# Performance work log

Hardware: AMD Instinct MI355X
Metric: run time of the kernel (lower is better)

## Reference

```python
import jax, jax.numpy as jnp
import numpy as np

# Grid shapes derived from video (T=30, H=720, W=1280), grid_size=8, n_levels=2:
# level i: ceil([T,H,W] / 8 / 2**i) + 1
GRID_SHAPES = [jnp.array([5.0, 91.0, 161.0], dtype=jnp.float32),
               jnp.array([3.0, 46.0, 81.0], dtype=jnp.float32)]
EMB_DIM = 16
N_PTS = 1048576
# 8 binary corner offsets of the unit cube, shape [8, 3]
OFFSET = jnp.array([[(i >> 2) & 1, (i >> 1) & 1, i & 1] for i in range(8)], dtype=jnp.float32)


def _encode_level(inputs, emb, grid_shape):
    # inputs: [N,3] in [0,1]; emb: [Gt,Gh,Gw,D]; grid_shape: [3] floats
    coords = inputs * (grid_shape - 1.0)                      # [N,3]
    corners = jnp.floor(OFFSET[None, :, :] + coords[:, None, :])  # [N,8,3]
    corners = jnp.clip(corners, 0.0, grid_shape - 1.0)        # [N,8,3]
    idx = corners.astype(jnp.int32)
    values = emb[idx[..., 0], idx[..., 1], idx[..., 2]]       # [N,8,D] gather
    w = 1.0 - jnp.abs(corners - coords[:, None, :])           # [N,8,3] trilinear
    w = jnp.prod(w, axis=-1, keepdims=True)                   # [N,8,1]
    return jnp.sum(w * values, axis=-2)                       # [N,D]


def setup_inputs() -> dict:
    key = jax.random.key(0)
    k1, k2, k3 = jax.random.split(key, 3)
    inputs = jax.random.uniform(k1, (N_PTS, 3), dtype=jnp.float32)
    emb0 = (jax.random.uniform(k2, (5, 91, 161, EMB_DIM), dtype=jnp.float32) * 2e-4 - 1e-4)
    emb1 = (jax.random.uniform(k3, (3, 46, 81, EMB_DIM), dtype=jnp.float32) * 2e-4 - 1e-4)
    return {"inputs": inputs, "emb0": emb0, "emb1": emb1}


def reference(inputs, emb0, emb1):
    out0 = _encode_level(inputs, emb0, GRID_SHAPES[0])
    out1 = _encode_level(inputs, emb1, GRID_SHAPES[1])
    # include_inputs=True -> concat raw coords first
    return jnp.concatenate([inputs, out0, out1], axis=-1)     # [N, 3 + 2*D]
```

## Files before the change

kernel.cpp:

```cpp
#include <hip/hip_runtime.h>

#define NPTS  1048576
#define BLOCK 256
#define PPB   128
#define D     16
#define ROW   35
#define CHUNK (PPB * ROW)

#define N0 (5 * 91 * 161 * 16)
#define N1 (3 * 46 * 81 * 16)
#define T8 ((N0 + N1) / 8)

#define SCALE   4096.0f
#define UNSCALE (1.0f / 4096.0f)

typedef float vf2 __attribute__((ext_vector_type(2)));

__global__ __launch_bounds__(256) void cvt_kernel(const float* __restrict__ e0,
                                                  const float* __restrict__ e1,
                                                  unsigned char* __restrict__ dst) {
    int i = blockIdx.x * 256 + threadIdx.x;
    if (i >= T8) return;
    int e = i * 8;
    const float* src = (e < N0) ? (e0 + e) : (e1 + (e - N0));
    float4 a = *(const float4*)(src);
    float4 b = *(const float4*)(src + 4);
    int w0 = __builtin_amdgcn_cvt_pk_fp8_f32(a.x * SCALE, a.y * SCALE, 0, false);
    w0     = __builtin_amdgcn_cvt_pk_fp8_f32(a.z * SCALE, a.w * SCALE, w0, true);
    int w1 = __builtin_amdgcn_cvt_pk_fp8_f32(b.x * SCALE, b.y * SCALE, 0, false);
    w1     = __builtin_amdgcn_cvt_pk_fp8_f32(b.z * SCALE, b.w * SCALE, w1, true);
    uint2 packed;
    packed.x = (unsigned int)w0;
    packed.y = (unsigned int)w1;
    *reinterpret_cast<uint2*>(dst + e) = packed;
}

template <int GT, int GH, int GW>
__device__ __forceinline__ void prep(float x, float y, float z, int h,
                                     int* __restrict__ off, float* __restrict__ w) {
    float ct = x * (float)(GT - 1);
    float ch = y * (float)(GH - 1);
    float cw = z * (float)(GW - 1);

    float ft0 = fminf(fmaxf(floorf(ct),       0.f), (float)(GT - 1));
    float ft1 = fminf(fmaxf(floorf(ct + 1.f), 0.f), (float)(GT - 1));
    float fh0 = fminf(fmaxf(floorf(ch),       0.f), (float)(GH - 1));
    float fh1 = fminf(fmaxf(floorf(ch + 1.f), 0.f), (float)(GH - 1));
    float fw0 = fminf(fmaxf(floorf(cw),       0.f), (float)(GW - 1));
    float fw1 = fminf(fmaxf(floorf(cw + 1.f), 0.f), (float)(GW - 1));

    float wt[2] = {1.f - fabsf(ft0 - ct), 1.f - fabsf(ft1 - ct)};
    float wh[2] = {1.f - fabsf(fh0 - ch), 1.f - fabsf(fh1 - ch)};
    float ww[2] = {1.f - fabsf(fw0 - cw), 1.f - fabsf(fw1 - cw)};
    int   it[2] = {(int)ft0, (int)ft1};
    int   ih[2] = {(int)fh0, (int)fh1};
    int   iw[2] = {(int)fw0, (int)fw1};

#pragma unroll
    for (int a = 0; a < 2; ++a)
#pragma unroll
        for (int b = 0; b < 2; ++b) {
            int rowbase = (it[a] * GH + ih[b]) * GW;
            float wab   = wt[a] * wh[b];
#pragma unroll
            for (int c = 0; c < 2; ++c) {
                int k  = a * 4 + b * 2 + c;
                off[k] = (rowbase + iw[c]) * D + h * 8;
                w[k]   = wab * ww[c];
            }
        }
}

__device__ __forceinline__ void accum8(uint2 v, float w, float* __restrict__ acc) {
    vf2 f01 = __builtin_amdgcn_cvt_pk_f32_fp8((int)v.x, false);
    vf2 f23 = __builtin_amdgcn_cvt_pk_f32_fp8((int)v.x, true);
    vf2 f45 = __builtin_amdgcn_cvt_pk_f32_fp8((int)v.y, false);
    vf2 f67 = __builtin_amdgcn_cvt_pk_f32_fp8((int)v.y, true);
    acc[0] = fmaf(w, f01.x, acc[0]);
    acc[1] = fmaf(w, f01.y, acc[1]);
    acc[2] = fmaf(w, f23.x, acc[2]);
    acc[3] = fmaf(w, f23.y, acc[3]);
    acc[4] = fmaf(w, f45.x, acc[4]);
    acc[5] = fmaf(w, f45.y, acc[5]);
    acc[6] = fmaf(w, f67.x, acc[6]);
    acc[7] = fmaf(w, f67.y, acc[7]);
}

__global__ __launch_bounds__(BLOCK) void mhe_kernel(
    const float* __restrict__ in,
    const unsigned char* __restrict__ e0,
    const unsigned char* __restrict__ e1,
    float* __restrict__ out)
{
    __shared__ float sin_[PPB * 3];
    __shared__ float sout[CHUNK];

    const int tid  = threadIdx.x;
    const int base = blockIdx.x * PPB;

    if (tid < PPB * 3 / 2) {
        reinterpret_cast<float2*>(sin_)[tid] =
            reinterpret_cast<const float2*>(in + (size_t)base * 3)[tid];
    }
    __syncthreads();

    const int p = tid >> 1;
    const int h = tid & 1;

    float x = sin_[p * 3 + 0];
    float y = sin_[p * 3 + 1];
    float z = sin_[p * 3 + 2];

    int   off0[8], off1[8];
    float w0[8],   w1[8];
    prep<5, 91, 161>(x, y, z, h, off0, w0);
    prep<3, 46, 81>(x, y, z, h, off1, w1);

    uint2 v0[8], v1[8];
#pragma unroll
    for (int k = 0; k < 8; ++k) v0[k] = *reinterpret_cast<const uint2*>(e0 + off0[k]);
#pragma unroll
    for (int k = 0; k < 8; ++k) v1[k] = *reinterpret_cast<const uint2*>(e1 + off1[k]);

    float a0[8] = {0,0,0,0,0,0,0,0};
    float a1[8] = {0,0,0,0,0,0,0,0};
#pragma unroll
    for (int k = 0; k < 8; ++k) accum8(v0[k], w0[k], a0);
#pragma unroll
    for (int k = 0; k < 8; ++k) accum8(v1[k], w1[k], a1);

    float* row = sout + p * ROW;
    if (h == 0) { row[0] = x; row[1] = y; row[2] = z; }
#pragma unroll
    for (int k = 0; k < 8; ++k) {
        row[3 + h * 8 + k]     = a0[k] * UNSCALE;
        row[3 + D + h * 8 + k] = a1[k] * UNSCALE;
    }
    __syncthreads();

    float4*       ob = reinterpret_cast<float4*>(out + (size_t)blockIdx.x * CHUNK);
    const float4* lb = reinterpret_cast<const float4*>(sout);
    for (int i = tid; i < CHUNK / 4; i += BLOCK) {
        ob[i] = lb[i];
    }
}

extern "C" void kernel_launch(void* const* d_in, const int* in_sizes, int n_in,
                              void* d_out, int out_size, void* d_ws, size_t ws_size,
                              hipStream_t stream) {
    const float* in   = (const float*)d_in[0];
    const float* emb0 = (const float*)d_in[1];
    const float* emb1 = (const float*)d_in[2];
    float*       out  = (float*)d_out;

    unsigned char* tbl = (unsigned char*)d_ws;

    cvt_kernel<<<(T8 + 255) / 256, 256, 0, stream>>>(emb0, emb1, tbl);
    mhe_kernel<<<NPTS / PPB, BLOCK, 0, stream>>>(in, tbl, tbl + N0, out);
}
```

Before: 183.5 us.

## Load both w-neighbor corners in one 16-byte gather and exchange halves via DPP

Each thread pair now issues 4 uint4 loads per level instead of 8 uint2 loads. Each load covers the two adjacent w-corners, clamping the base index to GW-2 so the pair stays in bounds. Lanes swap halves with a DPP quad-permute so each thread still accumulates its own 8 channels from both corners, and the w-weights are reassigned to match. Input loads and output stores also become nontemporal to cut cache pollution. The changes halve the number of gather instructions and the address math, at the cost of extra DPP moves and selects.

```diff
diff --git a/kernel.cpp b/kernel.cpp
--- a/kernel.cpp
+++ b/kernel.cpp
@@ -15,6 +15,7 @@
 #define UNSCALE (1.0f / 4096.0f)
 
 typedef float vf2 __attribute__((ext_vector_type(2)));
+typedef float vf4 __attribute__((ext_vector_type(4)));
 
 __global__ __launch_bounds__(256) void cvt_kernel(const float* __restrict__ e0,
                                                   const float* __restrict__ e1,
@@ -35,47 +36,50 @@
     *reinterpret_cast<uint2*>(dst + e) = packed;
 }
 
-template <int GT, int GH, int GW>
-__device__ __forceinline__ void prep(float x, float y, float z, int h,
-                                     int* __restrict__ off, float* __restrict__ w) {
+__device__ __forceinline__ unsigned swap1(unsigned v) {
+    return (unsigned)__builtin_amdgcn_update_dpp(0, (int)v, 0xB1, 0xF, 0xF, true);
+}
+
+template <int GT, int GU, int GW>
+__device__ __forceinline__ void prep2(float x, float y, float z, int h,
+                                      int* __restrict__ cb,
+                                      float* __restrict__ wtu,
+                                      float& wwn, float& wwf) {
     float ct = x * (float)(GT - 1);
-    float ch = y * (float)(GH - 1);
+    float cu = y * (float)(GU - 1);
     float cw = z * (float)(GW - 1);
 
-    float ft0 = fminf(fmaxf(floorf(ct),       0.f), (float)(GT - 1));
-    float ft1 = fminf(fmaxf(floorf(ct + 1.f), 0.f), (float)(GT - 1));
-    float fh0 = fminf(fmaxf(floorf(ch),       0.f), (float)(GH - 1));
-    float fh1 = fminf(fmaxf(floorf(ch + 1.f), 0.f), (float)(GH - 1));
-    float fw0 = fminf(fmaxf(floorf(cw),       0.f), (float)(GW - 1));
-    float fw1 = fminf(fmaxf(floorf(cw + 1.f), 0.f), (float)(GW - 1));
+    float t0 = floorf(ct), u0 = floorf(cu), w0 = floorf(cw);
+    float t1 = fminf(t0 + 1.f, (float)(GT - 1));
+    float u1 = fminf(u0 + 1.f, (float)(GU - 1));
+    float w1 = fminf(w0 + 1.f, (float)(GW - 1));
 
-    float wt[2] = {1.f - fabsf(ft0 - ct), 1.f - fabsf(ft1 - ct)};
-    float wh[2] = {1.f - fabsf(fh0 - ch), 1.f - fabsf(fh1 - ch)};
-    float ww[2] = {1.f - fabsf(fw0 - cw), 1.f - fabsf(fw1 - cw)};
-    int   it[2] = {(int)ft0, (int)ft1};
-    int   ih[2] = {(int)fh0, (int)fh1};
-    int   iw[2] = {(int)fw0, (int)fw1};
+    float wt[2] = {1.f - fabsf(t0 - ct), 1.f - fabsf(t1 - ct)};
+    float wu[2] = {1.f - fabsf(u0 - cu), 1.f - fabsf(u1 - cu)};
+    float ww0   = 1.f - fabsf(w0 - cw);
+    float ww1   = 1.f - fabsf(w1 - cw);
+    int   it[2] = {(int)t0, (int)t1};
+    int   iu[2] = {(int)u0, (int)u1};
+    int   iw0   = min((int)w0, GW - 2);
 
 #pragma unroll
     for (int a = 0; a < 2; ++a)
 #pragma unroll
         for (int b = 0; b < 2; ++b) {
-            int rowbase = (it[a] * GH + ih[b]) * GW;
-            float wab   = wt[a] * wh[b];
-#pragma unroll
-            for (int c = 0; c < 2; ++c) {
-                int k  = a * 4 + b * 2 + c;
-                off[k] = (rowbase + iw[c]) * D + h * 8;
-                w[k]   = wab * ww[c];
-            }
+            int k  = a * 2 + b;
+            cb[k]  = ((it[a] * GU + iu[b]) * GW + iw0 + h) * D;
+            wtu[k] = wt[a] * wu[b];
         }
+    wwn = h ? ww1 : ww0;
+    wwf = h ? ww0 : ww1;
 }
 
-__device__ __forceinline__ void accum8(uint2 v, float w, float* __restrict__ acc) {
-    vf2 f01 = __builtin_amdgcn_cvt_pk_f32_fp8((int)v.x, false);
-    vf2 f23 = __builtin_amdgcn_cvt_pk_f32_fp8((int)v.x, true);
-    vf2 f45 = __builtin_amdgcn_cvt_pk_f32_fp8((int)v.y, false);
-    vf2 f67 = __builtin_amdgcn_cvt_pk_f32_fp8((int)v.y, true);
+__device__ __forceinline__ void accum8w(unsigned d0, unsigned d1, float w,
+                                        float* __restrict__ acc) {
+    vf2 f01 = __builtin_amdgcn_cvt_pk_f32_fp8((int)d0, false);
+    vf2 f23 = __builtin_amdgcn_cvt_pk_f32_fp8((int)d0, true);
+    vf2 f45 = __builtin_amdgcn_cvt_pk_f32_fp8((int)d1, false);
+    vf2 f67 = __builtin_amdgcn_cvt_pk_f32_fp8((int)d1, true);
     acc[0] = fmaf(w, f01.x, acc[0]);
     acc[1] = fmaf(w, f01.y, acc[1]);
     acc[2] = fmaf(w, f23.x, acc[2]);
@@ -84,6 +88,23 @@
     acc[5] = fmaf(w, f45.y, acc[5]);
     acc[6] = fmaf(w, f67.x, acc[6]);
     acc[7] = fmaf(w, f67.y, acc[7]);
+}
+
+__device__ __forceinline__ void process4(const uint4* __restrict__ v,
+                                         const float* __restrict__ wtu,
+                                         float wwn, float wwf, int h,
+                                         float* __restrict__ acc) {
+#pragma unroll
+    for (int k = 0; k < 4; ++k) {
+        unsigned sx = swap1(v[k].x), sy = swap1(v[k].y);
+        unsigned sz = swap1(v[k].z), sw = swap1(v[k].w);
+        unsigned o0 = h ? v[k].z : v[k].x;
+        unsigned o1 = h ? v[k].w : v[k].y;
+        unsigned f0 = h ? sz : sx;
+        unsigned f1 = h ? sw : sy;
+        accum8w(o0, o1, wtu[k] * wwn, acc);
+        accum8w(f0, f1, wtu[k] * wwf, acc);
+    }
 }
 
 __global__ __launch_bounds__(BLOCK) void mhe_kernel(
@@ -99,8 +120,8 @@
     const int base = blockIdx.x * PPB;
 
     if (tid < PPB * 3 / 2) {
-        reinterpret_cast<float2*>(sin_)[tid] =
-            reinterpret_cast<const float2*>(in + (size_t)base * 3)[tid];
+        reinterpret_cast<vf2*>(sin_)[tid] = __builtin_nontemporal_load(
+            reinterpret_cast<const vf2*>(in + (size_t)base * 3) + tid);
     }
     __syncthreads();
 
@@ -111,23 +132,22 @@
     float y = sin_[p * 3 + 1];
     float z = sin_[p * 3 + 2];
 
-    int   off0[8], off1[8];
-    float w0[8],   w1[8];
-    prep<5, 91, 161>(x, y, z, h, off0, w0);
-    prep<3, 46, 81>(x, y, z, h, off1, w1);
+    int   cb0[4], cb1[4];
+    float wtu0[4], wtu1[4];
+    float wwn0, wwf0, wwn1, wwf1;
+    prep2<5, 91, 161>(x, y, z, h, cb0, wtu0, wwn0, wwf0);
+    prep2<3, 46, 81>(x, y, z, h, cb1, wtu1, wwn1, wwf1);
 
-    uint2 v0[8], v1[8];
+    uint4 v0[4], v1[4];
 #pragma unroll
-    for (int k = 0; k < 8; ++k) v0[k] = *reinterpret_cast<const uint2*>(e0 + off0[k]);
+    for (int k = 0; k < 4; ++k) v0[k] = *reinterpret_cast<const uint4*>(e0 + cb0[k]);
 #pragma unroll
-    for (int k = 0; k < 8; ++k) v1[k] = *reinterpret_cast<const uint2*>(e1 + off1[k]);
+    for (int k = 0; k < 4; ++k) v1[k] = *reinterpret_cast<const uint4*>(e1 + cb1[k]);
 
     float a0[8] = {0,0,0,0,0,0,0,0};
     float a1[8] = {0,0,0,0,0,0,0,0};
-#pragma unroll
-    for (int k = 0; k < 8; ++k) accum8(v0[k], w0[k], a0);
-#pragma unroll
-    for (int k = 0; k < 8; ++k) accum8(v1[k], w1[k], a1);
+    process4(v0, wtu0, wwn0, wwf0, h, a0);
+    process4(v1, wtu1, wwn1, wwf1, h, a1);
 
     float* row = sout + p * ROW;
     if (h == 0) { row[0] = x; row[1] = y; row[2] = z; }
@@ -138,10 +158,10 @@
     }
     __syncthreads();
 
-    float4*       ob = reinterpret_cast<float4*>(out + (size_t)blockIdx.x * CHUNK);
-    const float4* lb = reinterpret_cast<const float4*>(sout);
+    vf4*       ob = reinterpret_cast<vf4*>(out + (size_t)blockIdx.x * CHUNK);
+    const vf4* lb = reinterpret_cast<const vf4*>(sout);
     for (int i = tid; i < CHUNK / 4; i += BLOCK) {
-        ob[i] = lb[i];
+        __builtin_nontemporal_store(lb[i], ob + i);
     }
 }
 
```

Result: slower. 196.4 us (+7.0%).

## Store all 8 corners of each cell contiguously in FP8 table

Applied to the files above, without the earlier changes.

Builds a per-cell table holding all eight corner embeddings contiguously, 128 bytes per cell in FP8, so each thread issues four contiguous 16-byte loads instead of eight scattered 8-byte gathers. Boundary clipping is handled by clamping the cell index and folding the out-of-range corner's weight into the other corner. This trades an 8x-duplicated table (about 8.5MB, written once per call) and a heavier conversion kernel for fewer, coalesced gather transactions in the main kernel. Falls back to the old path if the workspace is too small.

```diff
diff --git a/kernel.cpp b/kernel.cpp
--- a/kernel.cpp
+++ b/kernel.cpp
@@ -11,10 +11,169 @@
 #define N1 (3 * 46 * 81 * 16)
 #define T8 ((N0 + N1) / 8)
 
+#define CELLS0 (4 * 90 * 160)
+#define CELLS1 (2 * 45 * 80)
+#define DUPSZ  ((size_t)(CELLS0 + CELLS1) * 128)
+#define TOT2   ((CELLS0 + CELLS1) * 2)
+
 #define SCALE   4096.0f
 #define UNSCALE (1.0f / 4096.0f)
 
 typedef float vf2 __attribute__((ext_vector_type(2)));
+
+
+template <int GT, int GU, int GW>
+__device__ __forceinline__ void expand_cell(const float* __restrict__ src,
+                                            int cid, int h,
+                                            unsigned char* __restrict__ dst) {
+    const int CW = GW - 1, CU = GU - 1;
+    int w = cid % CW;
+    int r = cid / CW;
+    int u = r % CU;
+    int t = r / CU;
+
+    uint2 arr[8];
+#pragma unroll
+    for (int k = 0; k < 8; ++k) {
+        int a = (k >> 2) & 1, b = (k >> 1) & 1, c = k & 1;
+        const float* s = src + ((size_t)((t + a) * GU + (u + b)) * GW + (w + c)) * D + h * 8;
+        float4 lo = *(const float4*)s;
+        float4 hi = *(const float4*)(s + 4);
+        int d0 = __builtin_amdgcn_cvt_pk_fp8_f32(lo.x * SCALE, lo.y * SCALE, 0, false);
+        d0     = __builtin_amdgcn_cvt_pk_fp8_f32(lo.z * SCALE, lo.w * SCALE, d0, true);
+        int d1 = __builtin_amdgcn_cvt_pk_fp8_f32(hi.x * SCALE, hi.y * SCALE, 0, false);
+        d1     = __builtin_amdgcn_cvt_pk_fp8_f32(hi.z * SCALE, hi.w * SCALE, d1, true);
+        arr[k].x = (unsigned)d0;
+        arr[k].y = (unsigned)d1;
+    }
+    uint4* o = (uint4*)(dst + (size_t)cid * 128 + h * 64);
+#pragma unroll
+    for (int j = 0; j < 4; ++j)
+        o[j] = make_uint4(arr[2 * j].x, arr[2 * j].y, arr[2 * j + 1].x, arr[2 * j + 1].y);
+}
+
+__global__ __launch_bounds__(256) void cvt2_kernel(const float* __restrict__ e0,
+                                                   const float* __restrict__ e1,
+                                                   unsigned char* __restrict__ dst) {
+    int i = blockIdx.x * 256 + threadIdx.x;
+    if (i >= TOT2) return;
+    int h   = i & 1;
+    int cid = i >> 1;
+    if (cid < CELLS0) expand_cell<5, 91, 161>(e0, cid, h, dst);
+    else              expand_cell<3, 46, 81>(e1, cid - CELLS0, h, dst + (size_t)CELLS0 * 128);
+}
+
+__device__ __forceinline__ void axisw(float x, float Gm1, float Gm2,
+                                      int& ic, float& wA, float& wB) {
+    float c  = x * Gm1;
+    float f0 = floorf(c);
+    float f1 = fminf(floorf(c + 1.f), Gm1);
+    float w0 = 1.f - fabsf(f0 - c);
+    float w1 = 1.f - fabsf(f1 - c);
+    float fc = fminf(f0, Gm2);
+    ic = (int)fc;
+    bool same = (f0 == fc);
+    wA = same ? w0 : 0.f;
+    wB = same ? w1 : (w0 + w1);
+}
+
+__device__ __forceinline__ void accum8w(unsigned d0, unsigned d1, float w,
+                                        float* __restrict__ acc) {
+    vf2 f01 = __builtin_amdgcn_cvt_pk_f32_fp8((int)d0, false);
+    vf2 f23 = __builtin_amdgcn_cvt_pk_f32_fp8((int)d0, true);
+    vf2 f45 = __builtin_amdgcn_cvt_pk_f32_fp8((int)d1, false);
+    vf2 f67 = __builtin_amdgcn_cvt_pk_f32_fp8((int)d1, true);
+    acc[0] = fmaf(w, f01.x, acc[0]);
+    acc[1] = fmaf(w, f01.y, acc[1]);
+    acc[2] = fmaf(w, f23.x, acc[2]);
+    acc[3] = fmaf(w, f23.y, acc[3]);
+    acc[4] = fmaf(w, f45.x, acc[4]);
+    acc[5] = fmaf(w, f45.y, acc[5]);
+    acc[6] = fmaf(w, f67.x, acc[6]);
+    acc[7] = fmaf(w, f67.y, acc[7]);
+}
+
+template <int GT, int GU, int GW>
+__device__ __forceinline__ void level2(float x, float y, float z, int h,
+                                       const unsigned char* __restrict__ tbl,
+                                       uint4* __restrict__ q,
+                                       float* __restrict__ wab,
+                                       float& wwA, float& wwB) {
+    int it, iu, iw;
+    float wtA, wtB, wuA, wuB;
+    axisw(x, (float)(GT - 1), (float)(GT - 2), it, wtA, wtB);
+    axisw(y, (float)(GU - 1), (float)(GU - 2), iu, wuA, wuB);
+    axisw(z, (float)(GW - 1), (float)(GW - 2), iw, wwA, wwB);
+    int cell = (it * (GU - 1) + iu) * (GW - 1) + iw;
+    const uint4* bp = (const uint4*)(tbl + (size_t)cell * 128 + (h << 6));
+#pragma unroll
+    for (int j = 0; j < 4; ++j) q[j] = bp[j];
+    wab[0] = wtA * wuA;
+    wab[1] = wtA * wuB;
+    wab[2] = wtB * wuA;
+    wab[3] = wtB * wuB;
+}
+
+__global__ __launch_bounds__(BLOCK) void mhe2_kernel(
+    const float* __restrict__ in,
+    const unsigned char* __restrict__ t0,
+    const unsigned char* __restrict__ t1,
+    float* __restrict__ out)
+{
+    __shared__ float sin_[PPB * 3];
+    __shared__ float sout[CHUNK];
+
+    const int tid  = threadIdx.x;
+    const int base = blockIdx.x * PPB;
+
+    if (tid < PPB * 3 / 2) {
+        reinterpret_cast<float2*>(sin_)[tid] =
+            reinterpret_cast<const float2*>(in + (size_t)base * 3)[tid];
+    }
+    __syncthreads();
+
+    const int p = tid >> 1;
+    const int h = tid & 1;
+
+    float x = sin_[p * 3 + 0];
+    float y = sin_[p * 3 + 1];
+    float z = sin_[p * 3 + 2];
+
+    uint4 q0[4], q1[4];
+    float wab0[4], wab1[4];
+    float wwA0, wwB0, wwA1, wwB1;
+    level2<5, 91, 161>(x, y, z, h, t0, q0, wab0, wwA0, wwB0);
+    level2<3, 46, 81>(x, y, z, h, t1, q1, wab1, wwA1, wwB1);
+
+    float a0[8] = {0,0,0,0,0,0,0,0};
+    float a1[8] = {0,0,0,0,0,0,0,0};
+#pragma unroll
+    for (int kp = 0; kp < 4; ++kp) {
+        accum8w(q0[kp].x, q0[kp].y, wab0[kp] * wwA0, a0);
+        accum8w(q0[kp].z, q0[kp].w, wab0[kp] * wwB0, a0);
+    }
+#pragma unroll
+    for (int kp = 0; kp < 4; ++kp) {
+        accum8w(q1[kp].x, q1[kp].y, wab1[kp] * wwA1, a1);
+        accum8w(q1[kp].z, q1[kp].w, wab1[kp] * wwB1, a1);
+    }
+
+    float* row = sout + p * ROW;
+    if (h == 0) { row[0] = x; row[1] = y; row[2] = z; }
+#pragma unroll
+    for (int k = 0; k < 8; ++k) {
+        row[3 + h * 8 + k]     = a0[k] * UNSCALE;
+        row[3 + D + h * 8 + k] = a1[k] * UNSCALE;
+    }
+    __syncthreads();
+
+    float4*       ob = reinterpret_cast<float4*>(out + (size_t)blockIdx.x * CHUNK);
+    const float4* lb = reinterpret_cast<const float4*>(sout);
+    for (int i = tid; i < CHUNK / 4; i += BLOCK) {
+        ob[i] = lb[i];
+    }
+}
+
 
 __global__ __launch_bounds__(256) void cvt_kernel(const float* __restrict__ e0,
                                                   const float* __restrict__ e1,
@@ -145,6 +304,7 @@
     }
 }
 
+
 extern "C" void kernel_launch(void* const* d_in, const int* in_sizes, int n_in,
                               void* d_out, int out_size, void* d_ws, size_t ws_size,
                               hipStream_t stream) {
@@ -155,6 +315,12 @@
 
     unsigned char* tbl = (unsigned char*)d_ws;
 
-    cvt_kernel<<<(T8 + 255) / 256, 256, 0, stream>>>(emb0, emb1, tbl);
-    mhe_kernel<<<NPTS / PPB, BLOCK, 0, stream>>>(in, tbl, tbl + N0, out);
-}
+    if (ws_size >= DUPSZ) {
+        cvt2_kernel<<<(TOT2 + 255) / 256, 256, 0, stream>>>(emb0, emb1, tbl);
+        mhe2_kernel<<<NPTS / PPB, BLOCK, 0, stream>>>(in, tbl,
+                                                      tbl + (size_t)CELLS0 * 128, out);
+    } else {
+        cvt_kernel<<<(T8 + 255) / 256, 256, 0, stream>>>(emb0, emb1, tbl);
+        mhe_kernel<<<NPTS / PPB, BLOCK, 0, stream>>>(in, tbl, tbl + N0, out);
+    }
+}
```

After: 188.2 us. 1.03x slower.
